# Performance work log

Measured on AMD Instinct MI355X. Metric: run time of the kernel, lower is better.

The kernel has to match this reference:

```python
import jax, jax.numpy as jnp
import numpy as np


def _sin_rpe(Lq, d_model, dtype):
    # sinusoidal relative-position embeddings for positions -(Lq-1)..(Lq-1)
    inv_freq = 1.0 / (10000.0 ** (jnp.arange(0, d_model, 2, dtype=jnp.float32) / d_model))
    pos = jnp.arange(-(Lq - 1), Lq, dtype=jnp.float32)  # [2Lq-1]
    ang = pos[:, None] * inv_freq[None, :]               # [2Lq-1, d_model/2]
    emb = jnp.zeros((2 * Lq - 1, d_model), dtype=jnp.float32)
    emb = emb.at[:, 0::2].set(jnp.sin(ang)).at[:, 1::2].set(jnp.cos(ang))
    return emb.astype(dtype)


def _rel_shift(x):
    # Transformer-XL relative shift. x: [B,H,Lq,Lr] with Lr = 2Lq-1
    B, H, Lq, Lr = x.shape
    xp = jnp.concatenate([jnp.zeros((B, H, Lq, 1), x.dtype), x], axis=-1)
    xp = xp.reshape(B, H, Lr + 1, Lq)
    return xp[:, :, 1:].reshape(B, H, Lq, Lr)[..., Lr - Lq:]


def setup_inputs() -> dict:
    key = jax.random.key(0)
    ks = jax.random.split(key, 7)
    B, Lq, D, H = 1, 2048, 1024, 16
    d_head = D // H
    s = 0.02
    return {
        "w": jax.random.normal(ks[0], (B, Lq, D), jnp.float32),
        "Wq": jax.random.normal(ks[1], (D, D), jnp.float32) * s,
        "Wk": jax.random.normal(ks[2], (D, D), jnp.float32) * s,
        "Wv": jax.random.normal(ks[3], (D, D), jnp.float32) * s,
        "Wr": jax.random.normal(ks[4], (D, D), jnp.float32) * s,
        "u_bias": jax.random.normal(ks[5], (H, d_head), jnp.float32) * 0.02,
        "v_bias": jax.random.normal(ks[6], (H, d_head), jnp.float32) * 0.02,
    }


def reference(w, Wq, Wk, Wv, Wr, u_bias, v_bias):
    B, Lq, D = w.shape
    H, d_head = u_bias.shape
    scale = 1.0 / np.sqrt(d_head).astype(np.float32)
    r = _sin_rpe(Lq, D, w.dtype)                          # [2Lq-1, D]
    # torch Linear: y = x @ W.T
    q = (w @ Wq.T).reshape(B, Lq, H, d_head).transpose(0, 2, 1, 3)  # [B,H,Lq,d]
    k = (w @ Wk.T).reshape(B, Lq, H, d_head).transpose(0, 2, 1, 3)
    v = (w @ Wv.T).reshape(B, Lq, H, d_head).transpose(0, 2, 1, 3)
    rp = (r @ Wr.T).reshape(2 * Lq - 1, H, d_head).transpose(1, 0, 2)  # [H,2Lq-1,d]
    AC = jnp.einsum('bhid,bhjd->bhij', q + u_bias[None, :, None, :], k)   # [B,H,Lq,Lq]
    BD = jnp.einsum('bhid,hjd->bhij', q + v_bias[None, :, None, :], rp)   # [B,H,Lq,2Lq-1]
    BD = _rel_shift(BD)                                                   # [B,H,Lq,Lq]
    attn = jax.nn.softmax((AC + BD) * scale, axis=-1)
    out = jnp.einsum('bhij,bhjd->bhid', attn, v)          # [B,H,Lq,d]
    return out.transpose(0, 2, 1, 3).reshape(B, Lq, D)
```

## Files before the change

### kernel.cpp

```cpp
#include <hip/hip_runtime.h>
#include <math.h>

#define LQ 2048
#define DM 1024
#define NH 16
#define DH 64
#define LR 4095

typedef __attribute__((ext_vector_type(4))) float f4v;
typedef __attribute__((ext_vector_type(8))) short s8v;
typedef __attribute__((ext_vector_type(2))) unsigned short us2;
typedef __attribute__((ext_vector_type(8))) unsigned short us8;
typedef __attribute__((ext_vector_type(2))) unsigned int u32x2;

__device__ __forceinline__ unsigned short f2bf(float x) {
    unsigned int u = __float_as_uint(x);
    return (unsigned short)((u + 0x7FFFu + ((u >> 16) & 1u)) >> 16);
}
__device__ __forceinline__ float bf2f(unsigned short s) {
    return __uint_as_float(((unsigned int)s) << 16);
}
__device__ __forceinline__ unsigned cvtpk(float lo, float hi) {
    unsigned r;
    asm("v_cvt_pk_bf16_f32 %0, %1, %2" : "=v"(r) : "v"(lo), "v"(hi));
    return r;
}
template<int CTRL>
__device__ __forceinline__ float rot16(float x) {
    return __uint_as_float((unsigned)__builtin_amdgcn_update_dpp(
        0, (int)__float_as_uint(x), CTRL, 0xF, 0xF, false));
}
#define GLOAD16(g, l) __builtin_amdgcn_global_load_lds((g), (l), 16, 0, 0)
#define WAVE_LDS_FENCE() do { \
    asm volatile("s_waitcnt lgkmcnt(0)" ::: "memory"); \
    __builtin_amdgcn_sched_barrier(0); } while (0)

__device__ __forceinline__ void sw_store8(unsigned short* base, int row, int c8, us8 v) {
    int byte = (row * 128 + c8 * 16) ^ ((row & 7) << 4);
    *(us8*)((char*)base + byte) = v;
}
__device__ __forceinline__ s8v sw_read8(const unsigned short* base, int row, int colshort) {
    int byte = (row * 128 + colshort * 2) ^ ((row & 7) << 4);
    return *(const s8v*)((const char*)base + byte);
}

__global__ __launch_bounds__(256)
void cast_all(const float* __restrict__ w, const float* __restrict__ Wq,
              const float* __restrict__ Wk, const float* __restrict__ Wv,
              const float* __restrict__ Wr, unsigned short* __restrict__ dst) {
    size_t e0 = ((size_t)blockIdx.x * 256 + threadIdx.x) * 8;
    const float* src;
    if (e0 < (size_t)LQ * DM) src = w + e0;
    else {
        size_t ro = e0 - (size_t)LQ * DM;
        int wi = (int)(ro >> 20);
        size_t off = ro & 1048575;
        src = (wi == 0 ? Wq : wi == 1 ? Wk : wi == 2 ? Wv : Wr) + off;
    }
    f4v a = *(const f4v*)src;
    f4v b = *(const f4v*)(src + 4);
    us8 o;
    o[0]=f2bf(a[0]); o[1]=f2bf(a[1]); o[2]=f2bf(a[2]); o[3]=f2bf(a[3]);
    o[4]=f2bf(b[0]); o[5]=f2bf(b[1]); o[6]=f2bf(b[2]); o[7]=f2bf(b[3]);
    *(us8*)(dst + e0) = o;
}

__global__ __launch_bounds__(256)
void r_kernel(unsigned short* __restrict__ r) {
    int tg = blockIdx.x * 256 + threadIdx.x;
    int gm = tg >> 9, c2 = tg & 511;
    float invf = expf(-(float)c2 * (9.210340371976184f / 512.0f));
    float ang = (float)(gm - (LQ - 1)) * invf;
    us2 o; o[0] = f2bf(sinf(ang)); o[1] = f2bf(cosf(ang));
    *(us2*)&r[(size_t)gm * DM + c2 * 2] = o;
}

__global__ __launch_bounds__(256)
void proj_gemm(const unsigned short* __restrict__ A,
               const unsigned short* __restrict__ b0, const unsigned short* __restrict__ b1,
               const unsigned short* __restrict__ b2,
               unsigned short* __restrict__ c0, unsigned short* __restrict__ c1,
               unsigned short* __restrict__ c2_, int M) {
    __shared__ unsigned short As[64 * 64];
    __shared__ unsigned short Bs[128 * 64];
    const int mat = blockIdx.y >> 3;
    const int m0 = blockIdx.x * 64, n0 = (blockIdx.y & 7) * 128;
    const unsigned short* B = mat == 0 ? b0 : mat == 1 ? b1 : b2;
    unsigned short* C = mat == 0 ? c0 : mat == 1 ? c1 : c2_;
    const int t = threadIdx.x;
    const int w = t >> 6, lan16 = t & 15, lgrp = (t & 63) >> 4;
    const int wm = (w >> 1) * 32, wn = (w & 1) * 64;
    f4v acc[2][4] = {};

    for (int k0 = 0; k0 < DM; k0 += 64) {
        #pragma unroll
        for (int it = 0; it < 2; ++it) {
            int slot = it * 256 + t;
            int row = slot >> 3, c8 = slot & 7;
            int gm = m0 + row; if (gm > M - 1) gm = M - 1;
            GLOAD16(A + (size_t)gm * DM + k0 + c8 * 8,
                    (char*)As + (size_t)(it * 256 + w * 64) * 16);
        }
        #pragma unroll
        for (int it = 0; it < 4; ++it) {
            int slot = it * 256 + t;
            int row = slot >> 3, c8 = slot & 7;
            GLOAD16(B + (size_t)(n0 + row) * DM + k0 + c8 * 8,
                    (char*)Bs + (size_t)(it * 256 + w * 64) * 16);
        }
        __syncthreads();
        #pragma unroll
        for (int kk = 0; kk < 2; ++kk) {
            s8v aF[2], bF[4];
            #pragma unroll
            for (int i = 0; i < 2; ++i)
                aF[i] = *(const s8v*)&As[(wm + i * 16 + lan16) * 64 + kk * 32 + lgrp * 8];
            #pragma unroll
            for (int j = 0; j < 4; ++j)
                bF[j] = *(const s8v*)&Bs[(wn + j * 16 + lan16) * 64 + kk * 32 + lgrp * 8];
            #pragma unroll
            for (int i = 0; i < 2; ++i)
                #pragma unroll
                for (int j = 0; j < 4; ++j)
                    acc[i][j] = __builtin_amdgcn_mfma_f32_16x16x32_bf16(aF[i], bF[j], acc[i][j], 0, 0, 0);
        }
        __syncthreads();
    }
    if (mat != 2) {
        #pragma unroll
        for (int i = 0; i < 2; ++i)
            #pragma unroll
            for (int j = 0; j < 4; ++j)
                #pragma unroll
                for (int rg = 0; rg < 4; ++rg) {
                    int row = m0 + wm + i * 16 + lgrp * 4 + rg;
                    if (row < M)
                        C[(size_t)row * DM + n0 + wn + j * 16 + lan16] = f2bf(acc[i][j][rg]);
                }
    } else {
        #pragma unroll
        for (int i = 0; i < 2; ++i)
            #pragma unroll
            for (int j = 0; j < 4; ++j) {
                int n = n0 + wn + j * 16 + lan16;
                int m = m0 + wm + i * 16 + lgrp * 4;
                u32x2 pp;
                pp[0] = cvtpk(acc[i][j][0], acc[i][j][1]);
                pp[1] = cvtpk(acc[i][j][2], acc[i][j][3]);
                *(u32x2*)&C[(size_t)n * LQ + m] = pp;
            }
    }
}

__global__ __launch_bounds__(256, 3)
void attn_mfma(const unsigned short* __restrict__ q, const unsigned short* __restrict__ kkg,
               const unsigned short* __restrict__ vtg, const unsigned short* __restrict__ rp,
               const float* __restrict__ ub, const float* __restrict__ vb,
               float* __restrict__ Oa, float* __restrict__ Ob,
               float* __restrict__ la, float* __restrict__ lb) {
    __shared__ unsigned short Ks[64 * 64];
    __shared__ unsigned short Vt[64 * 64];
    __shared__ unsigned short band[128 * 64];
    __shared__ unsigned short Gtw[4][80 * 18];
    __shared__ unsigned short Pt[4][64 * 18];

    const int dd = blockIdx.x;
    const int f = (dd & 7) * 128 + (dd >> 3);
    const int h = f >> 6;
    const int sp = (f >> 5) & 1;
    const int i0 = (f & 31) * 64;
    const int col0 = h * DH;
    float* Op = sp ? Ob : Oa;
    float* lp = sp ? lb : la;
    const int jbeg = sp * 1024;

    const int t = threadIdx.x;
    const int w = t >> 6, lan16 = t & 15, lgrp = (t & 63) >> 4;
    const int W = w * 16;
    const float C1 = 0.125f * 1.4426950408889634f;
    const float C0 = -4.0f * 1.4426950408889634f;

    unsigned short* gw = Gtw[w];
    unsigned short* pw = Pt[w];

    s8v quF[2], qvlF[2], qvsF[2];
    #pragma unroll
    for (int l = 0; l < 2; ++l) {
        int slot = l * 256 + t;
        int row = slot >> 3, c8 = slot & 7;
        us8 qv = *(const us8*)(q + (size_t)(i0 + row) * DM + col0 + c8 * 8);
        us8 o;
        #pragma unroll
        for (int i = 0; i < 8; ++i) o[i] = f2bf(bf2f(qv[i]) + ub[col0 + c8 * 8 + i]);
        *(us8*)&Ks[row * 64 + c8 * 8] = o;
    }
    __syncthreads();
    quF[0] = *(const s8v*)&Ks[(W + lan16) * 64 + lgrp * 8];
    quF[1] = *(const s8v*)&Ks[(W + lan16) * 64 + 32 + lgrp * 8];
    __syncthreads();
    #pragma unroll
    for (int l = 0; l < 3; ++l) {
        int slot = l * 256 + t;
        if (slot < 65 * 8) {
            int row = slot >> 3, c8 = slot & 7;
            int gi = i0 + row;
            us8 o = (us8){0,0,0,0,0,0,0,0};
            if (gi < LQ) {
                us8 qv = *(const us8*)(q + (size_t)gi * DM + col0 + c8 * 8);
                #pragma unroll
                for (int i = 0; i < 8; ++i) o[i] = f2bf(bf2f(qv[i]) + vb[col0 + c8 * 8 + i]);
            }
            *(us8*)&band[row * 64 + c8 * 8] = o;
        }
    }
    __syncthreads();
    qvlF[0] = *(const s8v*)&band[(W + lan16) * 64 + lgrp * 8];
    qvlF[1] = *(const s8v*)&band[(W + lan16) * 64 + 32 + lgrp * 8];
    qvsF[0] = *(const s8v*)&band[(W + 1 + lan16) * 64 + lgrp * 8];
    qvsF[1] = *(const s8v*)&band[(W + 1 + lan16) * 64 + 32 + lgrp * 8];

    f4v accO[4] = {};
    float lsum[4] = {0.f, 0.f, 0.f, 0.f};
    const int cbase = 48 - W;

    auto stage_band = [&](int base) {
        #pragma unroll
        for (int l = 0; l < 4; ++l) {
            int slot = l * 256 + t;
            int row = slot >> 3, c8 = slot & 7;
            int trow = base + row;
            us8 v = (us8){0,0,0,0,0,0,0,0};
            if (trow >= 0 && trow < LR)
                v = *(const us8*)(rp + (size_t)trow * DM + col0 + c8 * 8);
            sw_store8(band, row, c8, v);
        }
    };

    for (int tt = 0; tt < 16; ++tt) {
        const int j0 = jbeg + tt * 64;
        const int rel = j0 - i0;
        __syncthreads();
        #pragma unroll
        for (int l = 0; l < 2; ++l) {
            int slot = l * 256 + t;
            int row = slot >> 3, c8 = slot & 7;
            us8 v = *(const us8*)(kkg + (size_t)(j0 + row) * DM + col0 + c8 * 8);
            sw_store8(Ks, row, c8, v);
        }
        #pragma unroll
        for (int l = 0; l < 2; ++l) {
            int slot = l * 256 + t;
            int row = slot >> 3, c8 = slot & 7;
            us8 v = *(const us8*)(vtg + (size_t)(col0 + row) * LQ + j0 + c8 * 8);
            sw_store8(Vt, row, c8, v);
        }
        stage_band(rel <= 0 ? rel + 4031 : rel - 65);
        __syncthreads();

        f4v acF[4] = {};
        #pragma unroll
        for (int nf = 0; nf < 4; ++nf)
            #pragma unroll
            for (int kk = 0; kk < 2; ++kk) {
                s8v bF = sw_read8(Ks, nf * 16 + lan16, kk * 32 + lgrp * 8);
                acF[nf] = __builtin_amdgcn_mfma_f32_16x16x32_bf16(quF[kk], bF, acF[nf], 0, 0, 0);
            }
        f4v g[5] = {};
        auto gmm = [&](const s8v* qf) {
            #pragma unroll
            for (int c = 0; c < 5; ++c)
                #pragma unroll
                for (int kk = 0; kk < 2; ++kk) {
                    s8v bF = sw_read8(band, cbase + c * 16 + lan16, kk * 32 + lgrp * 8);
                    g[c] = __builtin_amdgcn_mfma_f32_16x16x32_bf16(qf[kk], bF, g[c], 0, 0, 0);
                }
        };
        if (rel <= 0) gmm(qvlF);
        else          gmm(qvsF);
        if (rel == 0) {
            __syncthreads();
            stage_band(-65);
            __syncthreads();
            gmm(qvsF);
        }
        #pragma unroll
        for (int c = 0; c < 5; ++c) {
            int cl = c * 16 + lan16;
            *(unsigned*)&gw[cl * 18 + lgrp * 4]     = cvtpk(g[c][0], g[c][1]);
            *(unsigned*)&gw[cl * 18 + lgrp * 4 + 2] = cvtpk(g[c][2], g[c][3]);
        }
        WAVE_LDS_FENCE();

        float p[4][4];
        #pragma unroll
        for (int rg = 0; rg < 4; ++rg) {
            const int rhat = lgrp * 4 + rg;
            #pragma unroll
            for (int nf = 0; nf < 4; ++nf) {
                int jl = nf * 16 + lan16;
                float bd = bf2f(gw[(jl - rhat + 15) * 18 + rhat]);
                float pp = exp2f(fmaf(acF[nf][rg] + bd, C1, C0));
                p[nf][rg] = pp;
                lsum[rg] += pp;
            }
        }
        #pragma unroll
        for (int nf = 0; nf < 4; ++nf) {
            int jl = nf * 16 + lan16;
            *(unsigned*)&pw[jl * 18 + lgrp * 4]     = cvtpk(p[nf][0], p[nf][1]);
            *(unsigned*)&pw[jl * 18 + lgrp * 4 + 2] = cvtpk(p[nf][2], p[nf][3]);
        }
        WAVE_LDS_FENCE();

        s8v pF[2];
        #pragma unroll
        for (int kk = 0; kk < 2; ++kk) {
            us8 tmp;
            #pragma unroll
            for (int e = 0; e < 8; ++e)
                tmp[e] = pw[(kk * 32 + lgrp * 8 + e) * 18 + lan16];
            pF[kk] = (s8v)tmp;
        }
        #pragma unroll
        for (int nf = 0; nf < 4; ++nf)
            #pragma unroll
            for (int kk = 0; kk < 2; ++kk) {
                s8v vF = sw_read8(Vt, nf * 16 + lan16, kk * 32 + lgrp * 8);
                accO[nf] = __builtin_amdgcn_mfma_f32_16x16x32_bf16(pF[kk], vF, accO[nf], 0, 0, 0);
            }
    }

    #pragma unroll
    for (int rg = 0; rg < 4; ++rg) {
        float s = lsum[rg];
        s += rot16<0x121>(s);
        s += rot16<0x122>(s);
        s += rot16<0x124>(s);
        s += rot16<0x128>(s);
        const int row = i0 + W + lgrp * 4 + rg;
        if (lan16 == 0) lp[h * LQ + row] = s;
        #pragma unroll
        for (int nf = 0; nf < 4; ++nf)
            Op[(size_t)row * DM + col0 + nf * 16 + lan16] = accO[nf][rg];
    }
}

__global__ __launch_bounds__(256)
void combine(const float* __restrict__ Oa, const float* __restrict__ Ob,
             const float* __restrict__ la, const float* __restrict__ lb,
             float* __restrict__ out) {
    int i = blockIdx.x * 256 + threadIdx.x;
    int e0 = i * 4;
    int row = e0 >> 10;
    int h = (e0 & 1023) >> 6;
    float inv = 1.f / (la[h * LQ + row] + lb[h * LQ + row]);
    f4v a = *(const f4v*)(Oa + e0);
    f4v b = *(const f4v*)(Ob + e0);
    f4v o = (a + b) * inv;
    *(f4v*)(out + e0) = o;
}

extern "C" void kernel_launch(void* const* d_in, const int* in_sizes, int n_in,
                              void* d_out, int out_size, void* d_ws, size_t ws_size,
                              hipStream_t stream) {
    const float* w  = (const float*)d_in[0];
    const float* Wq = (const float*)d_in[1];
    const float* Wk = (const float*)d_in[2];
    const float* Wv = (const float*)d_in[3];
    const float* Wr = (const float*)d_in[4];
    const float* ub = (const float*)d_in[5];
    const float* vb = (const float*)d_in[6];
    float* out = (float*)d_out;

    const size_t U = 1048576;
    unsigned short* ws = (unsigned short*)d_ws;
    unsigned short* wbf = ws;
    unsigned short* Wqb = ws + 2 * U;
    unsigned short* Wkb = ws + 3 * U;
    unsigned short* Wvb = ws + 4 * U;
    unsigned short* Wrb = ws + 5 * U;
    unsigned short* qb  = ws + 6 * U;
    unsigned short* kkb = ws + 8 * U;
    unsigned short* vtg = ws + 10 * U;
    unsigned short* rp  = ws + 12 * U;
    unsigned short* r   = ws + 16 * U;

    float* Oa = (float*)(ws + 16 * U);
    float* Ob = (float*)(ws);
    float* la = (float*)(ws + 4 * U);
    float* lb = la + NH * LQ;

    dim3 blk(256);
    hipLaunchKernelGGL(cast_all, dim3(3072), blk, 0, stream, w, Wq, Wk, Wv, Wr, wbf);
    hipLaunchKernelGGL(r_kernel, dim3(8190), blk, 0, stream, r);
    hipLaunchKernelGGL(proj_gemm, dim3(32, 24), blk, 0, stream,
                       wbf, Wqb, Wkb, Wvb, qb, kkb, vtg, LQ);
    hipLaunchKernelGGL(proj_gemm, dim3(64, 8), blk, 0, stream,
                       r, Wrb, Wrb, Wrb, rp, rp, rp, LR);
    hipLaunchKernelGGL(attn_mfma, dim3(1024), blk, 0, stream,
                       qb, kkb, vtg, rp, ub, vb, Oa, Ob, la, lb);
    hipLaunchKernelGGL(combine, dim3(2048), blk, 0, stream, Oa, Ob, la, lb, out);
}
```

Baseline: 146.8 us.

## Merge prep and projection launches; load attention operands directly from global

Folds the cast and sinusoidal-embedding kernels into one launch, and the QKV and R projections into one launch, cutting launch count from six to four. The attention kernel no longer stages K, V^T and the rel-pos band through shared memory with block barriers. Each wave instead reads MFMA fragments straight from global/L2, builds the q+bias fragments in registers, and raises the launch-bounds occupancy hint from 3 to 4. This removes syncthreads and LDS traffic but adds redundant global loads across waves and relies on cache hits for reuse.

```diff
diff --git a/kernel.cpp b/kernel.cpp
--- a/kernel.cpp
+++ b/kernel.cpp
@@ -12,6 +12,7 @@
 typedef __attribute__((ext_vector_type(2))) unsigned short us2;
 typedef __attribute__((ext_vector_type(8))) unsigned short us8;
 typedef __attribute__((ext_vector_type(2))) unsigned int u32x2;
+typedef __attribute__((ext_vector_type(4))) unsigned int u32x4;
 
 __device__ __forceinline__ unsigned short f2bf(float x) {
     unsigned int u = __float_as_uint(x);
@@ -35,58 +36,57 @@
     asm volatile("s_waitcnt lgkmcnt(0)" ::: "memory"); \
     __builtin_amdgcn_sched_barrier(0); } while (0)
 
-__device__ __forceinline__ void sw_store8(unsigned short* base, int row, int c8, us8 v) {
-    int byte = (row * 128 + c8 * 16) ^ ((row & 7) << 4);
-    *(us8*)((char*)base + byte) = v;
-}
-__device__ __forceinline__ s8v sw_read8(const unsigned short* base, int row, int colshort) {
-    int byte = (row * 128 + colshort * 2) ^ ((row & 7) << 4);
-    return *(const s8v*)((const char*)base + byte);
-}
+#define MFMA16(a, b, c) __builtin_amdgcn_mfma_f32_16x16x32_bf16((a), (b), (c), 0, 0, 0)
 
 __global__ __launch_bounds__(256)
-void cast_all(const float* __restrict__ w, const float* __restrict__ Wq,
-              const float* __restrict__ Wk, const float* __restrict__ Wv,
-              const float* __restrict__ Wr, unsigned short* __restrict__ dst) {
-    size_t e0 = ((size_t)blockIdx.x * 256 + threadIdx.x) * 8;
-    const float* src;
-    if (e0 < (size_t)LQ * DM) src = w + e0;
-    else {
-        size_t ro = e0 - (size_t)LQ * DM;
-        int wi = (int)(ro >> 20);
-        size_t off = ro & 1048575;
-        src = (wi == 0 ? Wq : wi == 1 ? Wk : wi == 2 ? Wv : Wr) + off;
-    }
-    f4v a = *(const f4v*)src;
-    f4v b = *(const f4v*)(src + 4);
-    us8 o;
-    o[0]=f2bf(a[0]); o[1]=f2bf(a[1]); o[2]=f2bf(a[2]); o[3]=f2bf(a[3]);
-    o[4]=f2bf(b[0]); o[5]=f2bf(b[1]); o[6]=f2bf(b[2]); o[7]=f2bf(b[3]);
-    *(us8*)(dst + e0) = o;
+void prep(const float* __restrict__ w, const float* __restrict__ Wq,
+          const float* __restrict__ Wk, const float* __restrict__ Wv,
+          const float* __restrict__ Wr, unsigned short* __restrict__ dst,
+          unsigned short* __restrict__ r) {
+    int b = blockIdx.x;
+    if (b < 3072) {
+        size_t e0 = ((size_t)b * 256 + threadIdx.x) * 8;
+        const float* src;
+        if (e0 < (size_t)LQ * DM) src = w + e0;
+        else {
+            size_t ro = e0 - (size_t)LQ * DM;
+            int wi = (int)(ro >> 20);
+            size_t off = ro & 1048575;
+            src = (wi == 0 ? Wq : wi == 1 ? Wk : wi == 2 ? Wv : Wr) + off;
+        }
+        f4v a = *(const f4v*)src;
+        f4v c = *(const f4v*)(src + 4);
+        us8 o;
+        o[0]=f2bf(a[0]); o[1]=f2bf(a[1]); o[2]=f2bf(a[2]); o[3]=f2bf(a[3]);
+        o[4]=f2bf(c[0]); o[5]=f2bf(c[1]); o[6]=f2bf(c[2]); o[7]=f2bf(c[3]);
+        *(us8*)(dst + e0) = o;
+    } else {
+        int tg = (b - 3072) * 256 + threadIdx.x;
+        int gm = tg >> 9, c2 = tg & 511;
+        float invf = expf(-(float)c2 * (9.210340371976184f / 512.0f));
+        float ang = (float)(gm - (LQ - 1)) * invf;
+        us2 o; o[0] = f2bf(sinf(ang)); o[1] = f2bf(cosf(ang));
+        *(us2*)&r[(size_t)gm * DM + c2 * 2] = o;
+    }
 }
 
 __global__ __launch_bounds__(256)
-void r_kernel(unsigned short* __restrict__ r) {
-    int tg = blockIdx.x * 256 + threadIdx.x;
-    int gm = tg >> 9, c2 = tg & 511;
-    float invf = expf(-(float)c2 * (9.210340371976184f / 512.0f));
-    float ang = (float)(gm - (LQ - 1)) * invf;
-    us2 o; o[0] = f2bf(sinf(ang)); o[1] = f2bf(cosf(ang));
-    *(us2*)&r[(size_t)gm * DM + c2 * 2] = o;
-}
-
-__global__ __launch_bounds__(256)
-void proj_gemm(const unsigned short* __restrict__ A,
-               const unsigned short* __restrict__ b0, const unsigned short* __restrict__ b1,
-               const unsigned short* __restrict__ b2,
-               unsigned short* __restrict__ c0, unsigned short* __restrict__ c1,
-               unsigned short* __restrict__ c2_, int M) {
+void proj_all(const unsigned short* __restrict__ wbf, const unsigned short* __restrict__ rr,
+              const unsigned short* __restrict__ Wqb, const unsigned short* __restrict__ Wkb,
+              const unsigned short* __restrict__ Wvb, const unsigned short* __restrict__ Wrb,
+              unsigned short* __restrict__ qb, unsigned short* __restrict__ kkb,
+              unsigned short* __restrict__ vtg, unsigned short* __restrict__ rp) {
     __shared__ unsigned short As[64 * 64];
     __shared__ unsigned short Bs[128 * 64];
-    const int mat = blockIdx.y >> 3;
-    const int m0 = blockIdx.x * 64, n0 = (blockIdx.y & 7) * 128;
-    const unsigned short* B = mat == 0 ? b0 : mat == 1 ? b1 : b2;
-    unsigned short* C = mat == 0 ? c0 : mat == 1 ? c1 : c2_;
+    int bid = blockIdx.x;
+    int mat, mblk, nblk;
+    if (bid < 768) { mat = bid >> 8; int rm = bid & 255; mblk = rm >> 3; nblk = rm & 7; }
+    else           { mat = 3; int rm = bid - 768; mblk = rm >> 3; nblk = rm & 7; }
+    const int M = (mat < 3) ? LQ : LR;
+    const unsigned short* A = (mat < 3) ? wbf : rr;
+    const unsigned short* B = mat == 0 ? Wqb : mat == 1 ? Wkb : mat == 2 ? Wvb : Wrb;
+    unsigned short* C = mat == 0 ? qb : mat == 1 ? kkb : mat == 2 ? vtg : rp;
+    const int m0 = mblk * 64, n0 = nblk * 128;
     const int t = threadIdx.x;
     const int w = t >> 6, lan16 = t & 15, lgrp = (t & 63) >> 4;
     const int wm = (w >> 1) * 32, wn = (w & 1) * 64;
@@ -122,7 +122,7 @@
             for (int i = 0; i < 2; ++i)
                 #pragma unroll
                 for (int j = 0; j < 4; ++j)
-                    acc[i][j] = __builtin_amdgcn_mfma_f32_16x16x32_bf16(aF[i], bF[j], acc[i][j], 0, 0, 0);
+                    acc[i][j] = MFMA16(aF[i], bF[j], acc[i][j]);
         }
         __syncthreads();
     }
@@ -152,15 +152,12 @@
     }
 }
 
-__global__ __launch_bounds__(256, 3)
+__global__ __launch_bounds__(256, 4)
 void attn_mfma(const unsigned short* __restrict__ q, const unsigned short* __restrict__ kkg,
                const unsigned short* __restrict__ vtg, const unsigned short* __restrict__ rp,
                const float* __restrict__ ub, const float* __restrict__ vb,
                float* __restrict__ Oa, float* __restrict__ Ob,
                float* __restrict__ la, float* __restrict__ lb) {
-    __shared__ unsigned short Ks[64 * 64];
-    __shared__ unsigned short Vt[64 * 64];
-    __shared__ unsigned short band[128 * 64];
     __shared__ unsigned short Gtw[4][80 * 18];
     __shared__ unsigned short Pt[4][64 * 18];
 
@@ -177,112 +174,71 @@
     const int t = threadIdx.x;
     const int w = t >> 6, lan16 = t & 15, lgrp = (t & 63) >> 4;
     const int W = w * 16;
+    const int cbase = 48 - W;
     const float C1 = 0.125f * 1.4426950408889634f;
     const float C0 = -4.0f * 1.4426950408889634f;
 
     unsigned short* gw = Gtw[w];
     unsigned short* pw = Pt[w];
 
+    union uv { u32x4 u; s8v s; };
+    auto mkfrag = [&](int gi, const float* bias, s8v* dstf) {
+        #pragma unroll
+        for (int kk = 0; kk < 2; ++kk) {
+            int cb = kk * 32 + lgrp * 8;
+            us8 qv = (us8){0,0,0,0,0,0,0,0};
+            if (gi < LQ) qv = *(const us8*)(q + (size_t)gi * DM + col0 + cb);
+            f4v b0 = *(const f4v*)(bias + col0 + cb);
+            f4v b1 = *(const f4v*)(bias + col0 + cb + 4);
+            uv o;
+            o.u[0] = cvtpk(bf2f(qv[0]) + b0[0], bf2f(qv[1]) + b0[1]);
+            o.u[1] = cvtpk(bf2f(qv[2]) + b0[2], bf2f(qv[3]) + b0[3]);
+            o.u[2] = cvtpk(bf2f(qv[4]) + b1[0], bf2f(qv[5]) + b1[1]);
+            o.u[3] = cvtpk(bf2f(qv[6]) + b1[2], bf2f(qv[7]) + b1[3]);
+            dstf[kk] = o.s;
+        }
+    };
     s8v quF[2], qvlF[2], qvsF[2];
-    #pragma unroll
-    for (int l = 0; l < 2; ++l) {
-        int slot = l * 256 + t;
-        int row = slot >> 3, c8 = slot & 7;
-        us8 qv = *(const us8*)(q + (size_t)(i0 + row) * DM + col0 + c8 * 8);
-        us8 o;
-        #pragma unroll
-        for (int i = 0; i < 8; ++i) o[i] = f2bf(bf2f(qv[i]) + ub[col0 + c8 * 8 + i]);
-        *(us8*)&Ks[row * 64 + c8 * 8] = o;
-    }
-    __syncthreads();
-    quF[0] = *(const s8v*)&Ks[(W + lan16) * 64 + lgrp * 8];
-    quF[1] = *(const s8v*)&Ks[(W + lan16) * 64 + 32 + lgrp * 8];
-    __syncthreads();
-    #pragma unroll
-    for (int l = 0; l < 3; ++l) {
-        int slot = l * 256 + t;
-        if (slot < 65 * 8) {
-            int row = slot >> 3, c8 = slot & 7;
-            int gi = i0 + row;
-            us8 o = (us8){0,0,0,0,0,0,0,0};
-            if (gi < LQ) {
-                us8 qv = *(const us8*)(q + (size_t)gi * DM + col0 + c8 * 8);
-                #pragma unroll
-                for (int i = 0; i < 8; ++i) o[i] = f2bf(bf2f(qv[i]) + vb[col0 + c8 * 8 + i]);
-            }
-            *(us8*)&band[row * 64 + c8 * 8] = o;
-        }
-    }
-    __syncthreads();
-    qvlF[0] = *(const s8v*)&band[(W + lan16) * 64 + lgrp * 8];
-    qvlF[1] = *(const s8v*)&band[(W + lan16) * 64 + 32 + lgrp * 8];
-    qvsF[0] = *(const s8v*)&band[(W + 1 + lan16) * 64 + lgrp * 8];
-    qvsF[1] = *(const s8v*)&band[(W + 1 + lan16) * 64 + 32 + lgrp * 8];
+    mkfrag(i0 + W + lan16, ub, quF);
+    mkfrag(i0 + W + lan16, vb, qvlF);
+    mkfrag(i0 + W + 1 + lan16, vb, qvsF);
 
     f4v accO[4] = {};
     float lsum[4] = {0.f, 0.f, 0.f, 0.f};
-    const int cbase = 48 - W;
-
-    auto stage_band = [&](int base) {
-        #pragma unroll
-        for (int l = 0; l < 4; ++l) {
-            int slot = l * 256 + t;
-            int row = slot >> 3, c8 = slot & 7;
-            int trow = base + row;
-            us8 v = (us8){0,0,0,0,0,0,0,0};
-            if (trow >= 0 && trow < LR)
-                v = *(const us8*)(rp + (size_t)trow * DM + col0 + c8 * 8);
-            sw_store8(band, row, c8, v);
-        }
-    };
 
     for (int tt = 0; tt < 16; ++tt) {
         const int j0 = jbeg + tt * 64;
         const int rel = j0 - i0;
-        __syncthreads();
-        #pragma unroll
-        for (int l = 0; l < 2; ++l) {
-            int slot = l * 256 + t;
-            int row = slot >> 3, c8 = slot & 7;
-            us8 v = *(const us8*)(kkg + (size_t)(j0 + row) * DM + col0 + c8 * 8);
-            sw_store8(Ks, row, c8, v);
-        }
-        #pragma unroll
-        for (int l = 0; l < 2; ++l) {
-            int slot = l * 256 + t;
-            int row = slot >> 3, c8 = slot & 7;
-            us8 v = *(const us8*)(vtg + (size_t)(col0 + row) * LQ + j0 + c8 * 8);
-            sw_store8(Vt, row, c8, v);
-        }
-        stage_band(rel <= 0 ? rel + 4031 : rel - 65);
-        __syncthreads();
 
         f4v acF[4] = {};
         #pragma unroll
-        for (int nf = 0; nf < 4; ++nf)
+        for (int nf = 0; nf < 4; ++nf) {
+            const unsigned short* kp = kkg + (size_t)(j0 + nf * 16 + lan16) * DM + col0;
             #pragma unroll
             for (int kk = 0; kk < 2; ++kk) {
-                s8v bF = sw_read8(Ks, nf * 16 + lan16, kk * 32 + lgrp * 8);
-                acF[nf] = __builtin_amdgcn_mfma_f32_16x16x32_bf16(quF[kk], bF, acF[nf], 0, 0, 0);
-            }
+                us8 bv = *(const us8*)(kp + kk * 32 + lgrp * 8);
+                acF[nf] = MFMA16(quF[kk], (s8v)bv, acF[nf]);
+            }
+        }
         f4v g[5] = {};
-        auto gmm = [&](const s8v* qf) {
-            #pragma unroll
-            for (int c = 0; c < 5; ++c)
+        auto bd_pass = [&](const s8v* qf, int base) {
+            #pragma unroll
+            for (int c = 0; c < 5; ++c) {
+                int trow = base + cbase + c * 16 + lan16;
+                bool ok = (trow >= 0) && (trow < LR);
+                const unsigned short* bp = rp + (size_t)trow * DM + col0;
                 #pragma unroll
                 for (int kk = 0; kk < 2; ++kk) {
-                    s8v bF = sw_read8(band, cbase + c * 16 + lan16, kk * 32 + lgrp * 8);
-                    g[c] = __builtin_amdgcn_mfma_f32_16x16x32_bf16(qf[kk], bF, g[c], 0, 0, 0);
+                    us8 bv = (us8){0,0,0,0,0,0,0,0};
+                    if (ok) bv = *(const us8*)(bp + kk * 32 + lgrp * 8);
+                    g[c] = MFMA16(qf[kk], (s8v)bv, g[c]);
                 }
+            }
         };
-        if (rel <= 0) gmm(qvlF);
-        else          gmm(qvsF);
-        if (rel == 0) {
-            __syncthreads();
-            stage_band(-65);
-            __syncthreads();
-            gmm(qvsF);
-        }
+        if (rel < 0)      bd_pass(qvlF, rel + 4031);
+        else if (rel > 0) bd_pass(qvsF, rel - 65);
+        else { bd_pass(qvlF, 4031); bd_pass(qvsF, -65); }
+
         #pragma unroll
         for (int c = 0; c < 5; ++c) {
             int cl = c * 16 + lan16;
@@ -291,24 +247,19 @@
         }
         WAVE_LDS_FENCE();
 
-        float p[4][4];
-        #pragma unroll
-        for (int rg = 0; rg < 4; ++rg) {
-            const int rhat = lgrp * 4 + rg;
-            #pragma unroll
-            for (int nf = 0; nf < 4; ++nf) {
-                int jl = nf * 16 + lan16;
-                float bd = bf2f(gw[(jl - rhat + 15) * 18 + rhat]);
-                float pp = exp2f(fmaf(acF[nf][rg] + bd, C1, C0));
-                p[nf][rg] = pp;
-                lsum[rg] += pp;
-            }
-        }
         #pragma unroll
         for (int nf = 0; nf < 4; ++nf) {
             int jl = nf * 16 + lan16;
-            *(unsigned*)&pw[jl * 18 + lgrp * 4]     = cvtpk(p[nf][0], p[nf][1]);
-            *(unsigned*)&pw[jl * 18 + lgrp * 4 + 2] = cvtpk(p[nf][2], p[nf][3]);
+            float pp[4];
+            #pragma unroll
+            for (int rg = 0; rg < 4; ++rg) {
+                const int rhat = lgrp * 4 + rg;
+                float bd = bf2f(gw[(jl - rhat + 15) * 18 + rhat]);
+                pp[rg] = exp2f(fmaf(acF[nf][rg] + bd, C1, C0));
+                lsum[rg] += pp[rg];
+            }
+            *(unsigned*)&pw[jl * 18 + lgrp * 4]     = cvtpk(pp[0], pp[1]);
+            *(unsigned*)&pw[jl * 18 + lgrp * 4 + 2] = cvtpk(pp[2], pp[3]);
         }
         WAVE_LDS_FENCE();
 
@@ -322,12 +273,14 @@
             pF[kk] = (s8v)tmp;
         }
         #pragma unroll
-        for (int nf = 0; nf < 4; ++nf)
+        for (int nf = 0; nf < 4; ++nf) {
+            const unsigned short* vp = vtg + (size_t)(col0 + nf * 16 + lan16) * LQ + j0;
             #pragma unroll
             for (int kk = 0; kk < 2; ++kk) {
-                s8v vF = sw_read8(Vt, nf * 16 + lan16, kk * 32 + lgrp * 8);
-                accO[nf] = __builtin_amdgcn_mfma_f32_16x16x32_bf16(pF[kk], vF, accO[nf], 0, 0, 0);
-            }
+                us8 bv = *(const us8*)(vp + kk * 32 + lgrp * 8);
+                accO[nf] = MFMA16(pF[kk], (s8v)bv, accO[nf]);
+            }
+        }
     }
 
     #pragma unroll
@@ -391,12 +344,9 @@
     float* lb = la + NH * LQ;
 
     dim3 blk(256);
-    hipLaunchKernelGGL(cast_all, dim3(3072), blk, 0, stream, w, Wq, Wk, Wv, Wr, wbf);
-    hipLaunchKernelGGL(r_kernel, dim3(8190), blk, 0, stream, r);
-    hipLaunchKernelGGL(proj_gemm, dim3(32, 24), blk, 0, stream,
-                       wbf, Wqb, Wkb, Wvb, qb, kkb, vtg, LQ);
-    hipLaunchKernelGGL(proj_gemm, dim3(64, 8), blk, 0, stream,
-                       r, Wrb, Wrb, Wrb, rp, rp, rp, LR);
+    hipLaunchKernelGGL(prep, dim3(11262), blk, 0, stream, w, Wq, Wk, Wv, Wr, wbf, r);
+    hipLaunchKernelGGL(proj_all, dim3(1280), blk, 0, stream,
+                       wbf, r, Wqb, Wkb, Wvb, Wrb, qb, kkb, vtg, rp);
     hipLaunchKernelGGL(attn_mfma, dim3(1024), blk, 0, stream,
                        qb, kkb, vtg, rp, ub, vb, Oa, Ob, la, lb);
     hipLaunchKernelGGL(combine, dim3(2048), blk, 0, stream, Oa, Ob, la, lb, out);
```

After: 280.7 us. 1.91x slower.
